# Performance work log

Measured on AMD Instinct MI355X. Metric: run time of the kernel, lower is better.

## Reference

```python
import jax, jax.numpy as jnp
import numpy as np


def setup_inputs() -> dict:
    key = jax.random.key(0)
    k1, k2, k3 = jax.random.split(key, 3)
    B, T, D, U = 64, 1024, 256, 256
    inputs = jax.random.normal(k1, (B, T, D), dtype=jnp.float32)
    W_xh = jax.random.normal(k2, (D, U), dtype=jnp.float32) * (1.0 / np.sqrt(D))
    W_hh = jax.random.normal(k3, (U, U), dtype=jnp.float32) * (1.0 / np.sqrt(U))
    b_h = jnp.zeros((U,), dtype=jnp.float32)
    return {"inputs": inputs, "W_xh": W_xh, "W_hh": W_hh, "b_h": b_h}


def reference(inputs, W_xh, W_hh, b_h):
    # inputs: [B, T, D]. Precompute input projection (same math as per-step matmul),
    # then scan the sequential recurrence: h_t = tanh(xW_t + h_{t-1} @ W_hh + b).
    B = inputs.shape[0]
    U = W_hh.shape[0]
    xW = jnp.einsum('btd,du->btu', inputs, W_xh) + b_h  # [B, T, U]
    h0 = jnp.zeros((B, U), dtype=inputs.dtype)

    def step(h, xw_t):
        h_new = jnp.tanh(xw_t + h @ W_hh)
        return h_new, h_new

    _, hs = jax.lax.scan(step, h0, jnp.swapaxes(xW, 0, 1))  # hs: [T, B, U]
    return jnp.swapaxes(hs, 0, 1)  # [B, T, U] (return_sequences=True)
```

## Files before the change

kernel.cpp:

```cpp
#include <hip/hip_runtime.h>
#include <math.h>

#define B_ 64
#define T_ 1024
#define D_ 256
#define U_ 256

typedef __fp16   hf2_t __attribute__((ext_vector_type(2)));
typedef _Float16 f16x8 __attribute__((ext_vector_type(8)));
typedef float    f32x4 __attribute__((ext_vector_type(4)));

__device__ __forceinline__ float fast_tanh2(float x) {
    float e = __expf(2.0f * x);
    return 1.0f - 2.0f * __builtin_amdgcn_rcpf(e + 1.0f);
}

#define CH_  16
#define NCH_ (T_ / CH_)
#define NT2_ 512

__global__ __launch_bounds__(NT2_) __attribute__((amdgpu_waves_per_eu(2, 2)))
void rnn_fused(const float* __restrict__ inputs,
               const float* __restrict__ W_xh,
               const float* __restrict__ W_hh,
               const float* __restrict__ b_h,
               float* __restrict__ out) {
    const int b    = (int)blockIdx.x;
    const int tid  = (int)threadIdx.x;
    const int w    = tid >> 6;
    const int lane = tid & 63;
    const int g    = lane >> 4;
    const int c    = lane & 15;
    const int n0   = w * 32;

    __shared__ float buf[2][CH_][U_];
    __shared__ __align__(16) _Float16 hl[2][U_];
    __shared__ __align__(16) _Float16 Ax[CH_ * D_];

    f16x8 whh[8][2], wxh[8][2];
    #pragma unroll
    for (int kt = 0; kt < 8; ++kt) {
        #pragma unroll
        for (int nt = 0; nt < 2; ++nt) {
            f16x8 vh, vx;
            #pragma unroll
            for (int j = 0; j < 8; ++j) {
                const int row = kt * 32 + g * 8 + j;
                const int col = n0 + nt * 16 + c;
                vh[j] = (_Float16)W_hh[(size_t)row * U_ + col];
                vx[j] = (_Float16)W_xh[(size_t)row * U_ + col];
            }
            whh[kt][nt] = vh;
            wxh[kt][nt] = vx;
        }
    }
    const float bb0 = b_h[n0 + c];
    const float bb1 = b_h[n0 + 16 + c];

    if (tid < 128) ((float*)&hl[0][0])[tid] = 0.f;

    const float* ibase = inputs + (size_t)b * T_ * D_;
    float* gbase = out + (size_t)b * T_ * U_;
    float* bufflat = &buf[0][0][0];

    const int srow = tid >> 5;
    const int sk8  = (tid & 31) * 8;
    char* const sdst = (char*)Ax + srow * 512 + ((sk8 * 2) ^ ((srow & 7) << 4));

    const int vbaseA = c * 512 + ((g * 16) ^ ((c & 7) << 4));

#define PACK8(DST, F0, F1)                                                    \
    {                                                                         \
        union { hf2_t p[4]; f16x8 v; } u;                                     \
        u.p[0] = __builtin_amdgcn_cvt_pkrtz((F0).x, (F0).y);                  \
        u.p[1] = __builtin_amdgcn_cvt_pkrtz((F0).z, (F0).w);                  \
        u.p[2] = __builtin_amdgcn_cvt_pkrtz((F1).x, (F1).y);                  \
        u.p[3] = __builtin_amdgcn_cvt_pkrtz((F1).z, (F1).w);                  \
        *(f16x8*)(DST) = u.v;                                                 \
    }

#define PROJECT(PB)                                                           \
    {                                                                         \
        f32x4 q0 = {0.f,0.f,0.f,0.f}, q1 = {0.f,0.f,0.f,0.f};                 \
        f32x4 q2 = {0.f,0.f,0.f,0.f}, q3 = {0.f,0.f,0.f,0.f};                 \
        _Pragma("unroll") for (int kt = 0; kt < 4; ++kt) {                    \
            f16x8 a = *(const f16x8*)((const char*)Ax + (vbaseA ^ (kt * 64)));\
            q0 = __builtin_amdgcn_mfma_f32_16x16x32_f16(a, wxh[kt][0], q0, 0, 0, 0); \
            q1 = __builtin_amdgcn_mfma_f32_16x16x32_f16(a, wxh[kt][1], q1, 0, 0, 0); \
        }                                                                     \
        _Pragma("unroll") for (int kt = 4; kt < 8; ++kt) {                    \
            f16x8 a = *(const f16x8*)((const char*)Ax + (vbaseA ^ (kt * 64)));\
            q2 = __builtin_amdgcn_mfma_f32_16x16x32_f16(a, wxh[kt][0], q2, 0, 0, 0); \
            q3 = __builtin_amdgcn_mfma_f32_16x16x32_f16(a, wxh[kt][1], q3, 0, 0, 0); \
        }                                                                     \
        _Pragma("unroll") for (int r = 0; r < 4; ++r) {                       \
            buf[PB][g * 4 + r][n0 + c]      = q0[r] + q2[r] + bb0;            \
            buf[PB][g * 4 + r][n0 + 16 + c] = q1[r] + q3[r] + bb1;            \
        }                                                                     \
    }

    {
        float4 f0 = *(const float4*)&ibase[8 * tid];
        float4 f1 = *(const float4*)&ibase[8 * tid + 4];
        PACK8(sdst, f0, f1)
    }
    __syncthreads();
    PROJECT(0)
    float4 p0, p1;
    {
        const float* gsrc = ibase + (size_t)CH_ * D_;
        p0 = *(const float4*)&gsrc[8 * tid];
        p1 = *(const float4*)&gsrc[8 * tid + 4];
    }
    asm volatile("s_waitcnt lgkmcnt(0)" ::: "memory");
    __builtin_amdgcn_s_barrier();
    asm volatile("" ::: "memory");

    const char* hrd = (const char*)&hl[0][0] + g * 16;
    char*       hwr = (char*)&hl[0][0] + (n0 + c) * 2;

#define STEP(J)                                                               \
    {                                                                         \
        const int RD = ((J) & 1) * 512;                                       \
        const int WR = 512 - RD;                                              \
        const float xw0 = *(const float*)(bufc + (J) * 1024);                 \
        const float xw1 = *(const float*)(bufc + (J) * 1024 + 64);            \
        f32x4 a0 = {0.f,0.f,0.f,0.f}, a1 = {0.f,0.f,0.f,0.f};                 \
        f32x4 c0 = {0.f,0.f,0.f,0.f}, c1 = {0.f,0.f,0.f,0.f};                 \
        _Pragma("unroll") for (int kt = 0; kt < 4; ++kt) {                    \
            f16x8 a = *(const f16x8*)(hrd + RD + 64 * kt);                    \
            a0 = __builtin_amdgcn_mfma_f32_16x16x32_f16(a, whh[kt][0], a0, 0, 0, 0); \
            a1 = __builtin_amdgcn_mfma_f32_16x16x32_f16(a, whh[kt][1], a1, 0, 0, 0); \
        }                                                                     \
        _Pragma("unroll") for (int kt = 4; kt < 8; ++kt) {                    \
            f16x8 a = *(const f16x8*)(hrd + RD + 64 * kt);                    \
            c0 = __builtin_amdgcn_mfma_f32_16x16x32_f16(a, whh[kt][0], c0, 0, 0, 0); \
            c1 = __builtin_amdgcn_mfma_f32_16x16x32_f16(a, whh[kt][1], c1, 0, 0, 0); \
        }                                                                     \
        const float h0 = fast_tanh2(a0[0] + c0[0] + xw0);                     \
        const float h1 = fast_tanh2(a1[0] + c1[0] + xw1);                     \
        if (g == 0) {                                                         \
            *(float*)(bufc + (J) * 1024)      = h0;                           \
            *(float*)(bufc + (J) * 1024 + 64) = h1;                           \
            *(_Float16*)(hwr + WR)      = (_Float16)h0;                       \
            *(_Float16*)(hwr + WR + 32) = (_Float16)h1;                       \
        }                                                                     \
        asm volatile("s_waitcnt lgkmcnt(0)" ::: "memory");                    \
        __builtin_amdgcn_s_barrier();                                         \
        asm volatile("" ::: "memory");                                        \
    }

    int cur = 0;
    for (int ch = 0; ch < NCH_; ++ch) {
        char* bufc = (char*)bufflat + cur * 16384 + (n0 + c) * 4;

        STEP(0)  STEP(1)  STEP(2)  STEP(3)
        STEP(4)  STEP(5)  STEP(6)  STEP(7)
        STEP(8)  STEP(9)  STEP(10) STEP(11)
        STEP(12) STEP(13) STEP(14) STEP(15)

        float4 d0 = *(const float4*)&bufflat[cur * 4096 + 8 * tid];
        float4 d1 = *(const float4*)&bufflat[cur * 4096 + 8 * tid + 4];

        if (ch + 1 < NCH_) PACK8(sdst, p0, p1)

        asm volatile("s_waitcnt lgkmcnt(0)" ::: "memory");
        __builtin_amdgcn_s_barrier();
        asm volatile("" ::: "memory");

        if (ch + 1 < NCH_) PROJECT(1 - cur)

        {
            float* gdst = gbase + (size_t)ch * CH_ * U_;
            *(float4*)&gdst[8 * tid]     = d0;
            *(float4*)&gdst[8 * tid + 4] = d1;
        }
        if (ch + 2 < NCH_) {
            const float* gsrc = ibase + (size_t)(ch + 2) * CH_ * D_;
            p0 = *(const float4*)&gsrc[8 * tid];
            p1 = *(const float4*)&gsrc[8 * tid + 4];
        }

        asm volatile("s_waitcnt lgkmcnt(0)" ::: "memory");
        __builtin_amdgcn_s_barrier();
        asm volatile("" ::: "memory");

        cur ^= 1;
    }
#undef STEP
#undef PROJECT
#undef PACK8
}

extern "C" void kernel_launch(void* const* d_in, const int* in_sizes, int n_in,
                              void* d_out, int out_size, void* d_ws, size_t ws_size,
                              hipStream_t stream) {
    const float* inputs = (const float*)d_in[0];
    const float* W_xh   = (const float*)d_in[1];
    const float* W_hh   = (const float*)d_in[2];
    const float* b_h    = (const float*)d_in[3];
    float* out = (float*)d_out;

    rnn_fused<<<B_, NT2_, 0, stream>>>(inputs, W_xh, W_hh, b_h, out);
}
```

Baseline: 580.1 us.

## Warp-specialize RNN kernel: scan waves and projection/store waves overlap per step

Splits the 8 waves into 4 scan waves that hold W_hh and run the recurrence over 64 columns each, and 4 helper waves that hold W_xh. The helper waves spread the next chunk's input projection, the output stores and the prefetch across the per-step barriers. This removes the two extra per-chunk barriers and the serialized projection between chunks. In exchange, each scan wave does twice the MFMA work per step on the critical path, and the two roles must stay in barrier lockstep.

```diff
diff --git a/kernel.cpp b/kernel.cpp
--- a/kernel.cpp
+++ b/kernel.cpp
@@ -31,43 +31,49 @@
     const int lane = tid & 63;
     const int g    = lane >> 4;
     const int c    = lane & 15;
-    const int n0   = w * 32;
+    const bool scanw   = (w < 4);
+    const int  colbase = (w & 3) * 64;
 
     __shared__ float buf[2][CH_][U_];
     __shared__ __align__(16) _Float16 hl[2][U_];
     __shared__ __align__(16) _Float16 Ax[CH_ * D_];
 
-    f16x8 whh[8][2], wxh[8][2];
+    const float* Wsrc = scanw ? W_hh : W_xh;
+    f16x8 wf[8][4];
     #pragma unroll
     for (int kt = 0; kt < 8; ++kt) {
         #pragma unroll
-        for (int nt = 0; nt < 2; ++nt) {
-            f16x8 vh, vx;
+        for (int nt = 0; nt < 4; ++nt) {
+            f16x8 v;
             #pragma unroll
-            for (int j = 0; j < 8; ++j) {
-                const int row = kt * 32 + g * 8 + j;
-                const int col = n0 + nt * 16 + c;
-                vh[j] = (_Float16)W_hh[(size_t)row * U_ + col];
-                vx[j] = (_Float16)W_xh[(size_t)row * U_ + col];
-            }
-            whh[kt][nt] = vh;
-            wxh[kt][nt] = vx;
-        }
-    }
-    const float bb0 = b_h[n0 + c];
-    const float bb1 = b_h[n0 + 16 + c];
+            for (int j = 0; j < 8; ++j)
+                v[j] = (_Float16)Wsrc[(size_t)(kt * 32 + g * 8 + j) * U_
+                                      + colbase + nt * 16 + c];
+            wf[kt][nt] = v;
+        }
+    }
+    float pbb0 = 0.f, pbb1 = 0.f, pbb2 = 0.f, pbb3 = 0.f;
+    if (!scanw) {
+        pbb0 = b_h[colbase + c];      pbb1 = b_h[colbase + 16 + c];
+        pbb2 = b_h[colbase + 32 + c]; pbb3 = b_h[colbase + 48 + c];
+    }
 
     if (tid < 128) ((float*)&hl[0][0])[tid] = 0.f;
 
     const float* ibase = inputs + (size_t)b * T_ * D_;
     float* gbase = out + (size_t)b * T_ * U_;
-    float* bufflat = &buf[0][0][0];
-
-    const int srow = tid >> 5;
-    const int sk8  = (tid & 31) * 8;
-    char* const sdst = (char*)Ax + srow * 512 + ((sk8 * 2) ^ ((srow & 7) << 4));
-
+    char*  bufD  = (char*)&buf[0][0][0];
+
+    const int pl = tid & 255;
+    const int srow = pl >> 5;
+    const int sk8b = (pl & 31) * 16;
+    char* const sdst0 = (char*)Ax + srow * 512 + (sk8b ^ ((srow & 7) << 4));
+    char* const sdst1 = sdst0 + 4096;
     const int vbaseA = c * 512 + ((g * 16) ^ ((c & 7) << 4));
+
+    float4 p0, p1, p2, p3;
+    f32x4 pacc0 = {0,0,0,0}, pacc1 = {0,0,0,0},
+          pacc2 = {0,0,0,0}, pacc3 = {0,0,0,0};
 
 #define PACK8(DST, F0, F1)                                                    \
     {                                                                         \
@@ -79,116 +85,149 @@
         *(f16x8*)(DST) = u.v;                                                 \
     }
 
-#define PROJECT(PB)                                                           \
-    {                                                                         \
-        f32x4 q0 = {0.f,0.f,0.f,0.f}, q1 = {0.f,0.f,0.f,0.f};                 \
-        f32x4 q2 = {0.f,0.f,0.f,0.f}, q3 = {0.f,0.f,0.f,0.f};                 \
-        _Pragma("unroll") for (int kt = 0; kt < 4; ++kt) {                    \
-            f16x8 a = *(const f16x8*)((const char*)Ax + (vbaseA ^ (kt * 64)));\
-            q0 = __builtin_amdgcn_mfma_f32_16x16x32_f16(a, wxh[kt][0], q0, 0, 0, 0); \
-            q1 = __builtin_amdgcn_mfma_f32_16x16x32_f16(a, wxh[kt][1], q1, 0, 0, 0); \
-        }                                                                     \
-        _Pragma("unroll") for (int kt = 4; kt < 8; ++kt) {                    \
-            f16x8 a = *(const f16x8*)((const char*)Ax + (vbaseA ^ (kt * 64)));\
-            q2 = __builtin_amdgcn_mfma_f32_16x16x32_f16(a, wxh[kt][0], q2, 0, 0, 0); \
-            q3 = __builtin_amdgcn_mfma_f32_16x16x32_f16(a, wxh[kt][1], q3, 0, 0, 0); \
-        }                                                                     \
-        _Pragma("unroll") for (int r = 0; r < 4; ++r) {                       \
-            buf[PB][g * 4 + r][n0 + c]      = q0[r] + q2[r] + bb0;            \
-            buf[PB][g * 4 + r][n0 + 16 + c] = q1[r] + q3[r] + bb1;            \
-        }                                                                     \
-    }
-
-    {
-        float4 f0 = *(const float4*)&ibase[8 * tid];
-        float4 f1 = *(const float4*)&ibase[8 * tid + 4];
-        PACK8(sdst, f0, f1)
+#define MFMA16(A, BF, ACC) \
+    ACC = __builtin_amdgcn_mfma_f32_16x16x32_f16((A), (BF), (ACC), 0, 0, 0)
+
+#define BAR()                                                                 \
+    asm volatile("s_waitcnt lgkmcnt(0)" ::: "memory");                        \
+    __builtin_amdgcn_s_barrier();                                             \
+    asm volatile("" ::: "memory");
+
+    if (!scanw) {
+        float4 f0 = *(const float4*)&ibase[8 * pl];
+        float4 f1 = *(const float4*)&ibase[8 * pl + 4];
+        float4 f2 = *(const float4*)&ibase[8 * pl + 2048];
+        float4 f3 = *(const float4*)&ibase[8 * pl + 2052];
+        PACK8(sdst0, f0, f1)
+        PACK8(sdst1, f2, f3)
     }
     __syncthreads();
-    PROJECT(0)
-    float4 p0, p1;
-    {
-        const float* gsrc = ibase + (size_t)CH_ * D_;
-        p0 = *(const float4*)&gsrc[8 * tid];
-        p1 = *(const float4*)&gsrc[8 * tid + 4];
-    }
-    asm volatile("s_waitcnt lgkmcnt(0)" ::: "memory");
-    __builtin_amdgcn_s_barrier();
-    asm volatile("" ::: "memory");
+    if (!scanw) {
+        #pragma unroll
+        for (int kt = 0; kt < 8; ++kt) {
+            f16x8 a = *(const f16x8*)((const char*)Ax + (vbaseA ^ (kt * 64)));
+            MFMA16(a, wf[kt][0], pacc0); MFMA16(a, wf[kt][1], pacc1);
+            MFMA16(a, wf[kt][2], pacc2); MFMA16(a, wf[kt][3], pacc3);
+        }
+        #pragma unroll
+        for (int r = 0; r < 4; ++r) {
+            float* row = &buf[0][g * 4 + r][colbase + c];
+            row[0]  = pacc0[r] + pbb0;  row[16] = pacc1[r] + pbb1;
+            row[32] = pacc2[r] + pbb2;  row[48] = pacc3[r] + pbb3;
+        }
+        pacc0 = f32x4{0,0,0,0}; pacc1 = f32x4{0,0,0,0};
+        pacc2 = f32x4{0,0,0,0}; pacc3 = f32x4{0,0,0,0};
+        const float* gs = ibase + (size_t)CH_ * D_;
+        p0 = *(const float4*)&gs[8 * pl];        p1 = *(const float4*)&gs[8 * pl + 4];
+        p2 = *(const float4*)&gs[8 * pl + 2048]; p3 = *(const float4*)&gs[8 * pl + 2052];
+    }
+    __syncthreads();
 
     const char* hrd = (const char*)&hl[0][0] + g * 16;
-    char*       hwr = (char*)&hl[0][0] + (n0 + c) * 2;
+    char*       hwr = (char*)&hl[0][0] + colbase * 2 + 2 * c;
 
 #define STEP(J)                                                               \
     {                                                                         \
         const int RD = ((J) & 1) * 512;                                       \
         const int WR = 512 - RD;                                              \
-        const float xw0 = *(const float*)(bufc + (J) * 1024);                 \
-        const float xw1 = *(const float*)(bufc + (J) * 1024 + 64);            \
-        f32x4 a0 = {0.f,0.f,0.f,0.f}, a1 = {0.f,0.f,0.f,0.f};                 \
-        f32x4 c0 = {0.f,0.f,0.f,0.f}, c1 = {0.f,0.f,0.f,0.f};                 \
+        char* bc = bufD + cur * 16384 + (J) * 1024 + (colbase + c) * 4;       \
+        const float xw0 = *(const float*)(bc);                                \
+        const float xw1 = *(const float*)(bc + 64);                           \
+        const float xw2 = *(const float*)(bc + 128);                          \
+        const float xw3 = *(const float*)(bc + 192);                          \
+        f32x4 ca0={0,0,0,0}, ca1={0,0,0,0}, ca2={0,0,0,0}, ca3={0,0,0,0};     \
+        f32x4 cb0={0,0,0,0}, cb1={0,0,0,0}, cb2={0,0,0,0}, cb3={0,0,0,0};     \
         _Pragma("unroll") for (int kt = 0; kt < 4; ++kt) {                    \
             f16x8 a = *(const f16x8*)(hrd + RD + 64 * kt);                    \
-            a0 = __builtin_amdgcn_mfma_f32_16x16x32_f16(a, whh[kt][0], a0, 0, 0, 0); \
-            a1 = __builtin_amdgcn_mfma_f32_16x16x32_f16(a, whh[kt][1], a1, 0, 0, 0); \
+            MFMA16(a, wf[kt][0], ca0); MFMA16(a, wf[kt][1], ca1);             \
+            MFMA16(a, wf[kt][2], ca2); MFMA16(a, wf[kt][3], ca3);             \
         }                                                                     \
         _Pragma("unroll") for (int kt = 4; kt < 8; ++kt) {                    \
             f16x8 a = *(const f16x8*)(hrd + RD + 64 * kt);                    \
-            c0 = __builtin_amdgcn_mfma_f32_16x16x32_f16(a, whh[kt][0], c0, 0, 0, 0); \
-            c1 = __builtin_amdgcn_mfma_f32_16x16x32_f16(a, whh[kt][1], c1, 0, 0, 0); \
-        }                                                                     \
-        const float h0 = fast_tanh2(a0[0] + c0[0] + xw0);                     \
-        const float h1 = fast_tanh2(a1[0] + c1[0] + xw1);                     \
+            MFMA16(a, wf[kt][0], cb0); MFMA16(a, wf[kt][1], cb1);             \
+            MFMA16(a, wf[kt][2], cb2); MFMA16(a, wf[kt][3], cb3);             \
+        }                                                                     \
+        const float h0 = fast_tanh2(ca0[0] + cb0[0] + xw0);                   \
+        const float h1 = fast_tanh2(ca1[0] + cb1[0] + xw1);                   \
+        const float h2 = fast_tanh2(ca2[0] + cb2[0] + xw2);                   \
+        const float h3 = fast_tanh2(ca3[0] + cb3[0] + xw3);                   \
         if (g == 0) {                                                         \
-            *(float*)(bufc + (J) * 1024)      = h0;                           \
-            *(float*)(bufc + (J) * 1024 + 64) = h1;                           \
+            *(float*)(bc)       = h0;  *(float*)(bc + 64)  = h1;              \
+            *(float*)(bc + 128) = h2;  *(float*)(bc + 192) = h3;              \
             *(_Float16*)(hwr + WR)      = (_Float16)h0;                       \
             *(_Float16*)(hwr + WR + 32) = (_Float16)h1;                       \
-        }                                                                     \
-        asm volatile("s_waitcnt lgkmcnt(0)" ::: "memory");                    \
-        __builtin_amdgcn_s_barrier();                                         \
-        asm volatile("" ::: "memory");                                        \
+            *(_Float16*)(hwr + WR + 64) = (_Float16)h2;                       \
+            *(_Float16*)(hwr + WR + 96) = (_Float16)h3;                       \
+        }                                                                     \
+        BAR()                                                                 \
+    }
+
+#define SLICE(J)                                                              \
+    {                                                                         \
+        if ((J) == 0) {                                                       \
+            if (ch > 0) {                                                     \
+                float v = *(const float*)(bufD + (1 - cur) * 16384            \
+                                          + 15 * 1024 + 4 * pl);              \
+                gbase[(size_t)(ch * 16 - 1) * 256 + pl] = v;                  \
+            }                                                                 \
+            if (ch + 1 < NCH_) { PACK8(sdst0, p0, p1) PACK8(sdst1, p2, p3) }  \
+        } else {                                                              \
+            float v = *(const float*)(bufD + cur * 16384                      \
+                                      + ((J) - 1) * 1024 + 4 * pl);           \
+            gbase[((size_t)ch * 16 + (J) - 1) * 256 + pl] = v;                \
+            if ((J) >= 1 && (J) <= 8 && ch + 1 < NCH_) {                      \
+                f16x8 a = *(const f16x8*)((const char*)Ax                     \
+                                          + (vbaseA ^ (((J) - 1) * 64)));     \
+                MFMA16(a, wf[(J) - 1][0], pacc0);                             \
+                MFMA16(a, wf[(J) - 1][1], pacc1);                             \
+                MFMA16(a, wf[(J) - 1][2], pacc2);                             \
+                MFMA16(a, wf[(J) - 1][3], pacc3);                             \
+            }                                                                 \
+            if ((J) == 9 && ch + 1 < NCH_) {                                  \
+                char* ob = bufD + (1 - cur) * 16384;                          \
+                _Pragma("unroll") for (int r = 0; r < 4; ++r) {               \
+                    float* row = (float*)(ob + (g * 4 + r) * 1024)            \
+                                 + colbase + c;                               \
+                    row[0]  = pacc0[r] + pbb0;  row[16] = pacc1[r] + pbb1;    \
+                    row[32] = pacc2[r] + pbb2;  row[48] = pacc3[r] + pbb3;    \
+                }                                                             \
+                pacc0 = f32x4{0,0,0,0}; pacc1 = f32x4{0,0,0,0};               \
+                pacc2 = f32x4{0,0,0,0}; pacc3 = f32x4{0,0,0,0};               \
+            }                                                                 \
+            if ((J) == 10 && ch + 2 < NCH_) {                                 \
+                const float* gs = ibase + (size_t)(ch + 2) * CH_ * D_;        \
+                p0 = *(const float4*)&gs[8 * pl];                             \
+                p1 = *(const float4*)&gs[8 * pl + 4];                         \
+                p2 = *(const float4*)&gs[8 * pl + 2048];                      \
+                p3 = *(const float4*)&gs[8 * pl + 2052];                      \
+            }                                                                 \
+        }                                                                     \
+        BAR()                                                                 \
     }
 
     int cur = 0;
     for (int ch = 0; ch < NCH_; ++ch) {
-        char* bufc = (char*)bufflat + cur * 16384 + (n0 + c) * 4;
-
-        STEP(0)  STEP(1)  STEP(2)  STEP(3)
-        STEP(4)  STEP(5)  STEP(6)  STEP(7)
-        STEP(8)  STEP(9)  STEP(10) STEP(11)
-        STEP(12) STEP(13) STEP(14) STEP(15)
-
-        float4 d0 = *(const float4*)&bufflat[cur * 4096 + 8 * tid];
-        float4 d1 = *(const float4*)&bufflat[cur * 4096 + 8 * tid + 4];
-
-        if (ch + 1 < NCH_) PACK8(sdst, p0, p1)
-
-        asm volatile("s_waitcnt lgkmcnt(0)" ::: "memory");
-        __builtin_amdgcn_s_barrier();
-        asm volatile("" ::: "memory");
-
-        if (ch + 1 < NCH_) PROJECT(1 - cur)
-
-        {
-            float* gdst = gbase + (size_t)ch * CH_ * U_;
-            *(float4*)&gdst[8 * tid]     = d0;
-            *(float4*)&gdst[8 * tid + 4] = d1;
-        }
-        if (ch + 2 < NCH_) {
-            const float* gsrc = ibase + (size_t)(ch + 2) * CH_ * D_;
-            p0 = *(const float4*)&gsrc[8 * tid];
-            p1 = *(const float4*)&gsrc[8 * tid + 4];
-        }
-
-        asm volatile("s_waitcnt lgkmcnt(0)" ::: "memory");
-        __builtin_amdgcn_s_barrier();
-        asm volatile("" ::: "memory");
-
+        if (scanw) {
+            STEP(0)  STEP(1)  STEP(2)  STEP(3)
+            STEP(4)  STEP(5)  STEP(6)  STEP(7)
+            STEP(8)  STEP(9)  STEP(10) STEP(11)
+            STEP(12) STEP(13) STEP(14) STEP(15)
+        } else {
+            SLICE(0)  SLICE(1)  SLICE(2)  SLICE(3)
+            SLICE(4)  SLICE(5)  SLICE(6)  SLICE(7)
+            SLICE(8)  SLICE(9)  SLICE(10) SLICE(11)
+            SLICE(12) SLICE(13) SLICE(14) SLICE(15)
+        }
         cur ^= 1;
     }
+    if (!scanw) {
+        float v = *(const float*)(bufD + 16384 + 15 * 1024 + 4 * pl);
+        gbase[(size_t)1023 * 256 + pl] = v;
+    }
 #undef STEP
-#undef PROJECT
+#undef SLICE
+#undef BAR
+#undef MFMA16
 #undef PACK8
 }
 
```

Result: slower. 650.4 us (+12.1%).
